# Kernel tuning notes

Hardware: AMD Instinct MI355X
Metric: run time of the kernel (lower is better)

Reference implementation:

```python
import jax, jax.numpy as jnp
import numpy as np

B, N, R = 4, 16, 64        # batch, permuted axis size, inner spatial size
M, S = N // 2, R * 2       # block count, block size


def _glorot(key, shape):
    fan_in, fan_out = shape[-2], shape[-1]
    lim = np.sqrt(6.0 / (fan_in + fan_out)).astype(np.float32)
    return jax.random.uniform(key, shape, jnp.float32, -lim, lim)


def setup_inputs() -> dict:
    key = jax.random.key(0)
    ks = jax.random.split(key, 10)
    inp = {
        "x": jax.random.normal(ks[0], (B, N, R, N, R, 2), jnp.float32),
        "perm_idx": jax.random.permutation(ks[1], N).astype(jnp.int32),
    }
    for i, name in enumerate(["hr1", "hi1", "hr2", "hi2", "hr3", "hi3", "hr4", "hi4"]):
        inp[name] = _glorot(ks[2 + i], (M, S, S))
    return inp


def _bilin(v, p_right, p_left):
    # v: (B, m, s, m, s). First contract the last s-axis against p_right's
    # block matmuls (block index = axis 3), then the axis-2 s-axis against
    # p_left's block matmuls (block index = axis 1).
    t = jnp.einsum('bmiaj,ajk->bmiak', v, p_right)
    return jnp.einsum('xbjci,bjk->xbkci', t, p_left)


def reference(x, perm_idx, hr1, hi1, hr2, hi2, hr3, hi3, hr4, hi4):
    m = x.shape[1] // 2
    s = x.shape[2] * 2
    n, r = m * 2, s // 2
    x = x.take(perm_idx, axis=1).take(perm_idx, axis=3)
    x = x.reshape((-1, m, s, m, s, 2))
    x_re, x_im = x[..., 0], x[..., 1]

    y_re = (_bilin(x_re, hr1, hr1) + _bilin(x_re, hi1, hi1)
            + _bilin(x_im, hi2, hr2) + _bilin(x_im, hr2, hi2))
    y_im = (_bilin(x_im, hr3, hr3) + _bilin(x_im, hi3, hi3)
            + _bilin(x_re, hi4, hr4) + _bilin(x_re, hr4, hi4))

    y = jnp.stack([y_re, y_im], axis=-1)
    return y.reshape((-1, n, r, n, r, 2))
```

## Files before the change

### kernel.cpp

```cpp
#include <hip/hip_runtime.h>
#include <hip/hip_bf16.h>
#include <stdint.h>

typedef __attribute__((ext_vector_type(8))) short bf16x8;
typedef __attribute__((ext_vector_type(4))) float f32x4;
typedef __attribute__((ext_vector_type(16))) float f32x16;

#define MFMA32(a, b, c) __builtin_amdgcn_mfma_f32_32x32x16_bf16((a), (b), (c), 0, 0, 0)

__device__ __forceinline__ unsigned short f2bf_rn(float f) {
    union { __bf16 b; unsigned short u; } v;
    v.b = (__bf16)f;
    return v.u;
}

__device__ __forceinline__ unsigned int pk2(float lo, float hi) {
    union { unsigned short s[2]; unsigned int u; } r;
    r.s[0] = f2bf_rn(lo); r.s[1] = f2bf_rn(hi);
    return r.u;
}

__device__ __forceinline__ void gload_lds16(const void* g, void* l) {
    __builtin_amdgcn_global_load_lds(
        (const __attribute__((address_space(1))) void*)g,
        (__attribute__((address_space(3))) void*)l, 16, 0, 0);
}

__global__ __launch_bounds__(256) void prep_h(
    const float* __restrict__ h0, const float* __restrict__ h1,
    const float* __restrict__ h2, const float* __restrict__ h3,
    const float* __restrict__ h4, const float* __restrict__ h5,
    const float* __restrict__ h6, const float* __restrict__ h7,
    unsigned short* __restrict__ ht)
{
    const float* hmap[8] = {h0, h1, h2, h3, h4, h5, h6, h7};
    const int wg = blockIdx.x;
    const int jblk = wg >> 2, qt = wg & 3;
    const float* src = hmap[jblk >> 3] + (jblk & 7) * 16384;
    unsigned short* dst = ht + jblk * 16384;
    __shared__ unsigned short tile[32 * 129];
    const int t = threadIdx.x;
    #pragma unroll
    for (int i = 0; i < 16; ++i) {
        int idx = t + 256 * i;
        int r = idx >> 5, kk = idx & 31;
        tile[kk * 129 + r] = f2bf_rn(src[r * 128 + qt * 32 + kk]);
    }
    __syncthreads();
    #pragma unroll
    for (int i = 0; i < 16; ++i) {
        int idx = t + 256 * i;
        int k = idx >> 7, r = idx & 127;
        dst[(qt * 32 + k) * 128 + r] = tile[k * 129 + r];
    }
}

__global__ __launch_bounds__(256, 1) void bilin_main(
    const float* __restrict__ x, const int* __restrict__ perm,
    const unsigned short* __restrict__ ht,
    unsigned short* __restrict__ ximws,
    float* __restrict__ out)
{
    const int wg = blockIdx.x;
    const int q = wg & 7, p = (wg >> 3) & 7, b = wg >> 6;
    const int tid = threadIdx.x;
    const int lane = tid & 63, wn = tid >> 6;
    const int l31 = lane & 31, hl = lane >> 5;

    __shared__ __align__(16) unsigned short smem[81920];
    unsigned short* xplane = smem;
    unsigned short* wre = smem + 16384;
    unsigned short* wim = smem + 32768;
    unsigned short* lre = smem + 49152;
    unsigned short* lim = smem + 65536;

    constexpr int pre_[4]  = {0, 1, 2, 3};
    constexpr int pim_[4]  = {6, 7, 4, 5};
    constexpr int rperm[8] = {0, 1, 3, 2, 4, 5, 7, 6};

    const int wubase = tid & ~63;
    auto stage_h = [&](unsigned short* dst, int blk) {
        const unsigned short* src = ht + blk * 16384;
        #pragma unroll
        for (int r = 0; r < 8; ++r) {
            const int idx = r * 256 + tid;
            const int row = idx >> 4, cin = idx & 15;
            gload_lds16(src + row * 128 + ((cin ^ (row & 15)) << 3),
                        dst + ((r * 256 + wubase) << 3));
        }
    };

    auto ldr = [&](const unsigned short* base, int row, int ch) -> bf16x8 {
        return *(const bf16x8*)(base + row * 128 + ((ch ^ (row & 15)) << 3));
    };

    unsigned short* myxim = ximws + (size_t)wg * 16384;

    auto stage_x_both = [&]() {
        #pragma unroll
        for (int i = 0; i < 8; ++i) {
            const int idx = i * 256 + tid;
            const int row = idx >> 4, cin = idx & 15;
            const int n1 = perm[2 * p + (row >> 6)];
            const int n2 = perm[2 * q + (cin >> 3)];
            const int r1 = row & 63, r2 = (cin & 7) * 8;
            const float* sp = x + ((size_t)((b * 16 + n1) * 64 + r1) * 1024
                                   + n2 * 64 + r2) * 2;
            float4 v0 = *(const float4*)(sp);
            float4 v1 = *(const float4*)(sp + 4);
            float4 v2 = *(const float4*)(sp + 8);
            float4 v3 = *(const float4*)(sp + 12);
            bf16x8 re, im;
            re[0] = (short)f2bf_rn(v0.x); re[1] = (short)f2bf_rn(v0.z);
            re[2] = (short)f2bf_rn(v1.x); re[3] = (short)f2bf_rn(v1.z);
            re[4] = (short)f2bf_rn(v2.x); re[5] = (short)f2bf_rn(v2.z);
            re[6] = (short)f2bf_rn(v3.x); re[7] = (short)f2bf_rn(v3.z);
            im[0] = (short)f2bf_rn(v0.y); im[1] = (short)f2bf_rn(v0.w);
            im[2] = (short)f2bf_rn(v1.y); im[3] = (short)f2bf_rn(v1.w);
            im[4] = (short)f2bf_rn(v2.y); im[5] = (short)f2bf_rn(v2.w);
            im[6] = (short)f2bf_rn(v3.y); im[7] = (short)f2bf_rn(v3.w);
            const int woff = row * 128 + ((cin ^ (row & 15)) << 3);
            *(bf16x8*)(xplane + woff) = re;
            *(bf16x8*)(myxim + woff) = im;
        }
    };

    auto restage_xim = [&]() {
        #pragma unroll
        for (int r = 0; r < 8; ++r) {
            const int idx = r * 256 + tid;
            gload_lds16(myxim + ((size_t)idx << 3),
                        xplane + ((r * 256 + wubase) << 3));
        }
    };

    bf16x8 xf[4][8];
    auto load_xf = [&]() {
        #pragma unroll
        for (int m2 = 0; m2 < 4; ++m2)
            #pragma unroll
            for (int ks = 0; ks < 8; ++ks)
                xf[m2][ks] = ldr(xplane, m2 * 32 + l31, 2 * ks + hl);
    };

    auto do_A = [&](const unsigned short* wb, f32x16 (&u)[4]) {
        bf16x8 wfr[8];
        #pragma unroll
        for (int ks = 0; ks < 8; ++ks)
            wfr[ks] = ldr(wb, wn * 32 + l31, 2 * ks + hl);
        #pragma unroll
        for (int m2 = 0; m2 < 4; ++m2)
            #pragma unroll
            for (int e = 0; e < 16; ++e) u[m2][e] = 0.f;
        #pragma unroll
        for (int ks = 0; ks < 8; ++ks)
            #pragma unroll
            for (int m2 = 0; m2 < 4; ++m2)
                u[m2] = MFMA32(xf[m2][ks], wfr[ks], u[m2]);
    };

    auto do_B = [&](const f32x16 (&u)[4], const unsigned short* lb,
                    f32x16 (&y)[4]) {
        union UF { unsigned int d[4]; bf16x8 v; };
        UF ufu[8];
        #pragma unroll
        for (int t = 0; t < 8; ++t) {
            const int f = t >> 1, qa = (t & 1) * 2, qb = qa + 1;
            unsigned int lo0 = pk2(u[f][4 * qa + 0], u[f][4 * qa + 1]);
            unsigned int lo1 = pk2(u[f][4 * qa + 2], u[f][4 * qa + 3]);
            unsigned int hi0 = pk2(u[f][4 * qb + 0], u[f][4 * qb + 1]);
            unsigned int hi1 = pk2(u[f][4 * qb + 2], u[f][4 * qb + 3]);
            unsigned int send0 = hl ? lo0 : hi0;
            unsigned int send1 = hl ? lo1 : hi1;
            unsigned int sx0 = (unsigned int)__shfl_xor((int)send0, 32);
            unsigned int sx1 = (unsigned int)__shfl_xor((int)send1, 32);
            ufu[t].d[0] = hl ? sx0 : lo0;
            ufu[t].d[1] = hl ? sx1 : lo1;
            ufu[t].d[2] = hl ? hi0 : sx0;
            ufu[t].d[3] = hl ? hi1 : sx1;
        }
        bf16x8 lcur[4], lnxt[4];
        #pragma unroll
        for (int mt = 0; mt < 4; ++mt)
            lcur[mt] = ldr(lb, mt * 32 + l31, hl);
        #pragma unroll
        for (int t = 0; t < 8; ++t) {
            if (t < 7) {
                #pragma unroll
                for (int mt = 0; mt < 4; ++mt)
                    lnxt[mt] = ldr(lb, mt * 32 + l31, 2 * (t + 1) + hl);
            }
            #pragma unroll
            for (int mt = 0; mt < 4; ++mt)
                y[mt] = MFMA32(lcur[mt], ufu[t].v, y[mt]);
            #pragma unroll
            for (int mt = 0; mt < 4; ++mt) lcur[mt] = lnxt[mt];
        }
    };

    stage_h(wre, rperm[pre_[0]] * 8 + q);
    stage_h(wim, rperm[pim_[0]] * 8 + q);
    stage_h(lre, pre_[0] * 8 + p);
    stage_h(lim, pim_[0] * 8 + p);
    stage_x_both();
    __syncthreads();
    load_xf();

    f32x16 yre[4], yim[4], u[4];
    #pragma unroll
    for (int i = 0; i < 4; ++i)
        #pragma unroll
        for (int e = 0; e < 16; ++e) { yre[i][e] = 0.f; yim[i][e] = 0.f; }

    #pragma unroll
    for (int ph = 0; ph < 4; ++ph) {
        do_A(wre, u);

        __syncthreads();
        if (ph < 3)
            stage_h(wre, rperm[pre_[ph + 1]] * 8 + q);
        if (ph == 0)
            restage_xim();

        do_B(u, lre, yre);
        do_A(wim, u);
        do_B(u, lim, yim);

        __syncthreads();
        if (ph < 3) {
            stage_h(wim, rperm[pim_[ph + 1]] * 8 + q);
            stage_h(lre, pre_[ph + 1] * 8 + p);
            stage_h(lim, pim_[ph + 1] * 8 + p);
        }
        if (ph == 1)
            load_xf();
    }

    float2* o2 = (float2*)out;
    #pragma unroll
    for (int mt = 0; mt < 4; ++mt)
        #pragma unroll
        for (int j = 0; j < 16; ++j) {
            const int row = mt * 32 + (j & 3) + 8 * (j >> 2) + 4 * hl;
            float2 v;
            v.x = yre[mt][j];
            v.y = yim[mt][j];
            o2[(size_t)(b * 1024 + p * 128 + row) * 1024
               + q * 128 + wn * 32 + l31] = v;
        }
}

extern "C" void kernel_launch(void* const* d_in, const int* in_sizes, int n_in,
                              void* d_out, int out_size, void* d_ws, size_t ws_size,
                              hipStream_t stream) {
    const float* x  = (const float*)d_in[0];
    const int* perm = (const int*)d_in[1];
    unsigned short* ws = (unsigned short*)d_ws;
    unsigned short* htp   = ws;
    unsigned short* ximws = ws + 1024u * 1024u;

    hipLaunchKernelGGL(prep_h, dim3(256), dim3(256), 0, stream,
        (const float*)d_in[2], (const float*)d_in[3], (const float*)d_in[4],
        (const float*)d_in[5], (const float*)d_in[6], (const float*)d_in[7],
        (const float*)d_in[8], (const float*)d_in[9], htp);
    hipLaunchKernelGGL(bilin_main, dim3(256), dim3(256), 0, stream,
        x, perm, htp, ximws, (float*)d_out);
}
```

Measured before the change: 42.21 us.

## Reorder phases to run both first-stage GEMMs before staging and second-stage GEMMs

Each phase now computes both the real and imaginary first-stage products and packs them to bf16 fragments up front. After a single barrier it issues the async LDS staging of the next phase's right-hand weights, then runs both second-stage MFMA passes. The left-hand weights for the current phase are staged at the start of the phase. The x imaginary-plane restage moves to phase 1. The explicit register double-buffering of left-weight fragments is dropped for direct loads. The aim is to overlap weight staging with more MFMA work and to use fewer barriers per phase. In exchange, register pressure rises from holding two packed fragment sets, and the left-weight staging now sits on the critical path at each phase start.

New measurement: 51.96 us. 23.1% more time.

```diff
diff --git a/kernel.cpp b/kernel.cpp
--- a/kernel.cpp
+++ b/kernel.cpp
@@ -7,6 +7,8 @@
 typedef __attribute__((ext_vector_type(16))) float f32x16;
 
 #define MFMA32(a, b, c) __builtin_amdgcn_mfma_f32_32x32x16_bf16((a), (b), (c), 0, 0, 0)
+
+union UF { unsigned int d[4]; bf16x8 v; };
 
 __device__ __forceinline__ unsigned short f2bf_rn(float f) {
     union { __bf16 b; unsigned short u; } v;
@@ -74,8 +76,8 @@
     unsigned short* lre = smem + 49152;
     unsigned short* lim = smem + 65536;
 
-    constexpr int pre_[4]  = {0, 1, 2, 3};
-    constexpr int pim_[4]  = {6, 7, 4, 5};
+    constexpr int pre_c[4] = {0, 1, 2, 3};
+    constexpr int pim_c[4] = {6, 7, 4, 5};
     constexpr int rperm[8] = {0, 1, 3, 2, 4, 5, 7, 6};
 
     const int wubase = tid & ~63;
@@ -159,10 +161,7 @@
                 u[m2] = MFMA32(xf[m2][ks], wfr[ks], u[m2]);
     };
 
-    auto do_B = [&](const f32x16 (&u)[4], const unsigned short* lb,
-                    f32x16 (&y)[4]) {
-        union UF { unsigned int d[4]; bf16x8 v; };
-        UF ufu[8];
+    auto build_ufu = [&](const f32x16 (&u)[4], UF (&ufu)[8]) {
         #pragma unroll
         for (int t = 0; t < 8; ++t) {
             const int f = t >> 1, qa = (t & 1) * 2, qb = qa + 1;
@@ -179,34 +178,27 @@
             ufu[t].d[2] = hl ? hi0 : sx0;
             ufu[t].d[3] = hl ? hi1 : sx1;
         }
-        bf16x8 lcur[4], lnxt[4];
-        #pragma unroll
-        for (int mt = 0; mt < 4; ++mt)
-            lcur[mt] = ldr(lb, mt * 32 + l31, hl);
+    };
+
+    auto do_Bgrid = [&](const UF (&ufu)[8], const unsigned short* lb,
+                        f32x16 (&y)[4]) {
         #pragma unroll
         for (int t = 0; t < 8; ++t) {
-            if (t < 7) {
-                #pragma unroll
-                for (int mt = 0; mt < 4; ++mt)
-                    lnxt[mt] = ldr(lb, mt * 32 + l31, 2 * (t + 1) + hl);
+            #pragma unroll
+            for (int mt = 0; mt < 4; ++mt) {
+                bf16x8 lfr = ldr(lb, mt * 32 + l31, 2 * t + hl);
+                y[mt] = MFMA32(lfr, ufu[t].v, y[mt]);
             }
-            #pragma unroll
-            for (int mt = 0; mt < 4; ++mt)
-                y[mt] = MFMA32(lcur[mt], ufu[t].v, y[mt]);
-            #pragma unroll
-            for (int mt = 0; mt < 4; ++mt) lcur[mt] = lnxt[mt];
-        }
-    };
-
-    stage_h(wre, rperm[pre_[0]] * 8 + q);
-    stage_h(wim, rperm[pim_[0]] * 8 + q);
-    stage_h(lre, pre_[0] * 8 + p);
-    stage_h(lim, pim_[0] * 8 + p);
+        }
+    };
+
+    stage_h(wre, rperm[pre_c[0]] * 8 + q);
+    stage_h(wim, rperm[pim_c[0]] * 8 + q);
     stage_x_both();
     __syncthreads();
     load_xf();
 
-    f32x16 yre[4], yim[4], u[4];
+    f32x16 yre[4], yim[4];
     #pragma unroll
     for (int i = 0; i < 4; ++i)
         #pragma unroll
@@ -214,26 +206,31 @@
 
     #pragma unroll
     for (int ph = 0; ph < 4; ++ph) {
+        stage_h(lre, pre_c[ph] * 8 + p);
+        stage_h(lim, pim_c[ph] * 8 + p);
+        if (ph == 1)
+            restage_xim();
+
+        f32x16 u[4];
+        UF ufu_re[8], ufu_im[8];
         do_A(wre, u);
+        build_ufu(u, ufu_re);
+        do_A(wim, u);
+        build_ufu(u, ufu_im);
 
         __syncthreads();
-        if (ph < 3)
-            stage_h(wre, rperm[pre_[ph + 1]] * 8 + q);
-        if (ph == 0)
-            restage_xim();
-
-        do_B(u, lre, yre);
-        do_A(wim, u);
-        do_B(u, lim, yim);
-
-        __syncthreads();
+
         if (ph < 3) {
-            stage_h(wim, rperm[pim_[ph + 1]] * 8 + q);
-            stage_h(lre, pre_[ph + 1] * 8 + p);
-            stage_h(lim, pim_[ph + 1] * 8 + p);
+            stage_h(wre, rperm[pre_c[ph + 1]] * 8 + q);
+            stage_h(wim, rperm[pim_c[ph + 1]] * 8 + q);
         }
         if (ph == 1)
             load_xf();
+
+        do_Bgrid(ufu_re, lre, yre);
+        do_Bgrid(ufu_im, lim, yim);
+
+        __syncthreads();
     }
 
     float2* o2 = (float2*)out;
```

## Double-buffer weight and left-factor tiles across an eight-step unified block loop

Applied to the files above, without the earlier changes.

Replaces the four-phase loop, with its separate re and im weight and left buffers, by an eight-step loop over a combined block sequence. Two ping-pong buffer pairs hold the weight and left-factor tiles, and the next step's tiles are staged at the start of the current step. This lets the global-to-LDS loads overlap a full A+B compute step, with one barrier per step. The output accumulator (re or im) is chosen per step, and the x_re to x_im plane switch is rescheduled to match the new order.

Result: faster. 40.02 us (-5.2%).

```diff
diff --git a/kernel.cpp b/kernel.cpp
--- a/kernel.cpp
+++ b/kernel.cpp
@@ -69,13 +69,8 @@
 
     __shared__ __align__(16) unsigned short smem[81920];
     unsigned short* xplane = smem;
-    unsigned short* wre = smem + 16384;
-    unsigned short* wim = smem + 32768;
-    unsigned short* lre = smem + 49152;
-    unsigned short* lim = smem + 65536;
-
-    constexpr int pre_[4]  = {0, 1, 2, 3};
-    constexpr int pim_[4]  = {6, 7, 4, 5};
+
+    constexpr int cseq[8]  = {0, 1, 6, 7, 2, 3, 4, 5};
     constexpr int rperm[8] = {0, 1, 3, 2, 4, 5, 7, 6};
 
     const int wubase = tid & ~63;
@@ -143,11 +138,38 @@
                 xf[m2][ks] = ldr(xplane, m2 * 32 + l31, 2 * ks + hl);
     };
 
-    auto do_A = [&](const unsigned short* wb, f32x16 (&u)[4]) {
+    stage_h(smem + 16384, rperm[cseq[0]] * 8 + q);
+    stage_h(smem + 49152, cseq[0] * 8 + p);
+    stage_x_both();
+    __syncthreads();
+    load_xf();
+
+    f32x16 yre[4], yim[4];
+    #pragma unroll
+    for (int i = 0; i < 4; ++i) {
+        #pragma unroll
+        for (int e = 0; e < 16; ++e) { yre[i][e] = 0.f; yim[i][e] = 0.f; }
+    }
+
+    #pragma unroll
+    for (int cc = 0; cc < 8; ++cc) {
+        const unsigned short* wb = smem + 16384 + (cc & 1) * 16384;
+        const unsigned short* lb = smem + 49152 + (cc & 1) * 16384;
+
+        if (cc < 7) {
+            stage_h(smem + 16384 + ((cc + 1) & 1) * 16384,
+                    rperm[cseq[cc + 1]] * 8 + q);
+            stage_h(smem + 49152 + ((cc + 1) & 1) * 16384,
+                    cseq[cc + 1] * 8 + p);
+        }
+        if (cc == 1)
+            restage_xim();
+
         bf16x8 wfr[8];
         #pragma unroll
         for (int ks = 0; ks < 8; ++ks)
             wfr[ks] = ldr(wb, wn * 32 + l31, 2 * ks + hl);
+        f32x16 u[4];
         #pragma unroll
         for (int m2 = 0; m2 < 4; ++m2)
             #pragma unroll
@@ -157,10 +179,9 @@
             #pragma unroll
             for (int m2 = 0; m2 < 4; ++m2)
                 u[m2] = MFMA32(xf[m2][ks], wfr[ks], u[m2]);
-    };
-
-    auto do_B = [&](const f32x16 (&u)[4], const unsigned short* lb,
-                    f32x16 (&y)[4]) {
+
+        if (cc == 3) load_xf();
+
         union UF { unsigned int d[4]; bf16x8 v; };
         UF ufu[8];
         #pragma unroll
@@ -190,50 +211,17 @@
                 for (int mt = 0; mt < 4; ++mt)
                     lnxt[mt] = ldr(lb, mt * 32 + l31, 2 * (t + 1) + hl);
             }
-            #pragma unroll
-            for (int mt = 0; mt < 4; ++mt)
-                y[mt] = MFMA32(lcur[mt], ufu[t].v, y[mt]);
+            const bool isRe = (cc & 3) < 2;
+            #pragma unroll
+            for (int mt = 0; mt < 4; ++mt) {
+                if (isRe) yre[mt] = MFMA32(lcur[mt], ufu[t].v, yre[mt]);
+                else      yim[mt] = MFMA32(lcur[mt], ufu[t].v, yim[mt]);
+            }
             #pragma unroll
             for (int mt = 0; mt < 4; ++mt) lcur[mt] = lnxt[mt];
         }
-    };
-
-    stage_h(wre, rperm[pre_[0]] * 8 + q);
-    stage_h(wim, rperm[pim_[0]] * 8 + q);
-    stage_h(lre, pre_[0] * 8 + p);
-    stage_h(lim, pim_[0] * 8 + p);
-    stage_x_both();
-    __syncthreads();
-    load_xf();
-
-    f32x16 yre[4], yim[4], u[4];
-    #pragma unroll
-    for (int i = 0; i < 4; ++i)
-        #pragma unroll
-        for (int e = 0; e < 16; ++e) { yre[i][e] = 0.f; yim[i][e] = 0.f; }
-
-    #pragma unroll
-    for (int ph = 0; ph < 4; ++ph) {
-        do_A(wre, u);
 
         __syncthreads();
-        if (ph < 3)
-            stage_h(wre, rperm[pre_[ph + 1]] * 8 + q);
-        if (ph == 0)
-            restage_xim();
-
-        do_B(u, lre, yre);
-        do_A(wim, u);
-        do_B(u, lim, yim);
-
-        __syncthreads();
-        if (ph < 3) {
-            stage_h(wim, rperm[pim_[ph + 1]] * 8 + q);
-            stage_h(lre, pre_[ph + 1] * 8 + p);
-            stage_h(lim, pim_[ph + 1] * 8 + p);
-        }
-        if (ph == 1)
-            load_xf();
     }
 
     float2* o2 = (float2*)out;
```
